# Optimization experiments

Measured on AMD Instinct MI355X. Metric: run time of the kernel, lower is better.

The kernel has to match this reference:

```python
import jax, jax.numpy as jnp
import numpy as np


def _lstm_layer(x, W_ih, W_hh, b_ih, b_hh, reverse=False):
    """Single LSTM layer. x: [T, B, D] -> outputs [T, B, H]. PyTorch gate order i,f,g,o."""
    H = W_hh.shape[-1]
    B = x.shape[1]
    # precompute input contribution for all steps
    xg = jnp.einsum('tbd,gd->tbg', x, W_ih) + b_ih + b_hh  # [T, B, 4H]

    def step(carry, xt):
        h, c = carry
        gates = xt + h @ W_hh.T
        i, f, g, o = jnp.split(gates, 4, axis=-1)
        c = jax.nn.sigmoid(f) * c + jax.nn.sigmoid(i) * jnp.tanh(g)
        h = jax.nn.sigmoid(o) * jnp.tanh(c)
        return (h, c), h

    init = (jnp.zeros((B, H), x.dtype), jnp.zeros((B, H), x.dtype))
    _, hs = jax.lax.scan(step, init, xg, reverse=reverse)
    return hs


def setup_inputs() -> dict:
    key = jax.random.key(0)
    ks = jax.random.split(key, 24)
    B, S, L = 64, 256, 16
    VOCAB, CVOCAB, NCLS = 50000, 128, 50
    E, CE, H = 100, 50, 300
    IN0 = E + CE          # 150, bilstm layer-0 input
    IN1 = 2 * H           # 600, bilstm layer-1 input

    def u(k, shape, fan):
        lim = 1.0 / np.sqrt(fan)
        return jax.random.uniform(k, shape, jnp.float32, -lim, lim)

    inp = {
        'word_ids': jax.random.randint(ks[0], (B, S), 0, VOCAB, jnp.int32),
        'char_ids': jax.random.randint(ks[1], (B, S, L), 0, CVOCAB, jnp.int32),
        'word_embed': jax.random.normal(ks[2], (VOCAB, E), jnp.float32) * 0.1,
        'char_embed': jax.random.normal(ks[3], (CVOCAB, CE), jnp.float32) * 0.1,
        # char LSTM: 2 layers, unidirectional, input==hidden==CE -> stack over layers
        'cWih': u(ks[4], (2, 4 * CE, CE), CE),
        'cWhh': u(ks[5], (2, 4 * CE, CE), CE),
        'cbih': u(ks[6], (2, 4 * CE), CE),
        'cbhh': u(ks[7], (2, 4 * CE), CE),
        # bilstm layer 0: stack over directions [2, ...]
        'b0_Wih': u(ks[8], (2, 4 * H, IN0), H),
        'b0_Whh': u(ks[9], (2, 4 * H, H), H),
        'b0_bih': u(ks[10], (2, 4 * H), H),
        'b0_bhh': u(ks[11], (2, 4 * H), H),
        # bilstm layer 1
        'b1_Wih': u(ks[12], (2, 4 * H, IN1), H),
        'b1_Whh': u(ks[13], (2, 4 * H, H), H),
        'b1_bih': u(ks[14], (2, 4 * H), H),
        'b1_bhh': u(ks[15], (2, 4 * H), H),
        'fcW': u(ks[16], (NCLS, 2 * H), 2 * H),
        'fcb': u(ks[17], (NCLS,), 2 * H),
    }
    return inp


def reference(word_ids, char_ids, word_embed, char_embed, cWih, cWhh, cbih, cbhh,
              b0_Wih, b0_Whh, b0_bih, b0_bhh, b1_Wih, b1_Whh, b1_bih, b1_bhh,
              fcW, fcb):
    B, S, L = char_ids.shape
    CE = char_embed.shape[1]

    # --- char-level path: batch all B*S words through the 2-layer char LSTM ---
    ch = char_embed[char_ids.reshape(B * S, L)]            # [BS, L, CE]
    x = jnp.transpose(ch, (1, 0, 2))                       # [L, BS, CE]
    x = _lstm_layer(x, cWih[0], cWhh[0], cbih[0], cbhh[0])
    x = _lstm_layer(x, cWih[1], cWhh[1], cbih[1], cbhh[1])
    char_feat = x[-1].reshape(B, S, CE)                    # last step of top layer

    # --- word path + concat ---
    emb = word_embed[word_ids]                             # [B, S, E]
    seq = jnp.transpose(jnp.concatenate([emb, char_feat], axis=-1), (1, 0, 2))  # [S, B, 150]

    # --- 2-layer bidirectional LSTM ---
    f0 = _lstm_layer(seq, b0_Wih[0], b0_Whh[0], b0_bih[0], b0_bhh[0])
    r0 = _lstm_layer(seq, b0_Wih[1], b0_Whh[1], b0_bih[1], b0_bhh[1], reverse=True)
    h0 = jnp.concatenate([f0, r0], axis=-1)                # [S, B, 600]
    f1 = _lstm_layer(h0, b1_Wih[0], b1_Whh[0], b1_bih[0], b1_bhh[0])
    r1 = _lstm_layer(h0, b1_Wih[1], b1_Whh[1], b1_bih[1], b1_bhh[1], reverse=True)
    h1 = jnp.concatenate([f1, r1], axis=-1)                # [S, B, 600]

    out = jnp.einsum('sbh,ch->bsc', h1, fcW) + fcb         # [B, S, NCLS]
    return jax.nn.log_softmax(out, axis=-1)
```

## Files before the change

### kernel.cpp

```cpp
#include <hip/hip_runtime.h>

typedef unsigned short u16;
typedef unsigned int   u32;
typedef unsigned long long u64;
typedef __attribute__((ext_vector_type(8))) short bf16x8;
typedef __attribute__((ext_vector_type(4))) float f32x4;

#define MFMA16(a,b,c) __builtin_amdgcn_mfma_f32_16x16x32_bf16((a),(b),(c),0,0,0)

#define NWG   19
#define HP    320
#define GP    304
#define XGB   4096
#define SLOTS 257
#define HSLOT 20480

static const size_t OFF_XG  = 0;
static const size_t SZ_XG   = (size_t)2*256*NWG*XGB*2;
static const size_t OFF_H0  = OFF_XG + SZ_XG;
static const size_t SZ_HB   = (size_t)2*SLOTS*HSLOT*2;
static const size_t OFF_H1  = OFF_H0 + SZ_HB;
static const size_t OFF_CF  = OFF_H1 + SZ_HB;
static const size_t SZ_CF   = (size_t)16384*64*2;
static const size_t OFF_W0  = OFF_CF + SZ_CF;
static const size_t SZ_W0   = (size_t)2432*160*2;
static const size_t OFF_W1  = OFF_W0 + SZ_W0;
static const size_t SZ_W1   = (size_t)2432*640*2;
static const size_t OFF_WFC = OFF_W1 + SZ_W1;
static const size_t SZ_WFC  = (size_t)64*640*2;
static const size_t OFF_B0  = OFF_WFC + SZ_WFC;
static const size_t OFF_B1  = OFF_B0 + 2432*4;
static const size_t OFF_BFC = OFF_B1 + 2432*4;
static const size_t OFF_DT  = OFF_BFC + 64*4;
static const size_t WS_NEED = OFF_DT + 4;

__device__ __forceinline__ float bf2f(u16 u){ union{u32 i; float f;} v; v.i=(u32)u<<16; return v.f; }
__device__ __forceinline__ u16 f2bf(float f){ union{float f; u32 u;} v; v.f=f; u32 r=v.u+0x7fffu+((v.u>>16)&1u); return (u16)(r>>16); }
__device__ __forceinline__ float sigf(float x){ return __builtin_amdgcn_rcpf(1.f+__builtin_amdgcn_exp2f(-1.4426950408889634f*x)); }
__device__ __forceinline__ float tanhf_(float x){ return 2.f*__builtin_amdgcn_rcpf(1.f+__builtin_amdgcn_exp2f(-2.8853900817779268f*x))-1.f; }
__device__ __forceinline__ float ldf(const void* p, size_t i, bool f32){
  return f32 ? ((const float*)p)[i] : bf2f(((const u16*)p)[i]);
}
__device__ __forceinline__ u16 ldh(const void* p, size_t i, bool f32){
  return f32 ? f2bf(((const float*)p)[i]) : ((const u16*)p)[i];
}

__global__ __launch_bounds__(256,1) void k_detect(const u16* __restrict__ probe, u32* __restrict__ cnt)
{
  int c = 0;
  for (int i = threadIdx.x; i < 65536; i += 256) {
    u16 v = probe[i];
    if (((v >> 7) & 0xFF) == 0xFF) ++c;
  }
  if (c) atomicAdd(cnt, (u32)c);
}

__global__ __launch_bounds__(256,4) void k_prep(
    const void* __restrict__ b0_Wih, const void* __restrict__ b0_bih, const void* __restrict__ b0_bhh,
    const void* __restrict__ b1_Wih, const void* __restrict__ b1_bih, const void* __restrict__ b1_bhh,
    const void* __restrict__ fcW,    const void* __restrict__ fcb,
    u16* __restrict__ W0p, u16* __restrict__ W1p, u16* __restrict__ Wfc,
    float* __restrict__ bias0, float* __restrict__ bias1, float* __restrict__ biasfc,
    const u32* __restrict__ dtf)
{
  const bool isf32 = (*dtf >= 8u);
  const int T0 = 2432*160, T1 = 2432*640, T2 = 64*640;
  const int total = T0 + T1 + T2 + 2432 + 2432 + 64;
  for (int i = blockIdx.x*256 + threadIdx.x; i < total; i += gridDim.x*256) {
    int x = i;
    if (x < T0) {
      int n = x/160, k = x%160;
      int dir = n/1216, cc = n%1216, g = cc/GP, uu = cc%GP;
      W0p[x] = (uu<300 && k<150) ? ldh(b0_Wih, ((size_t)dir*1200 + g*300 + uu)*150 + k, isf32) : (u16)0;
      continue;
    }
    x -= T0;
    if (x < T1) {
      int n = x/640, k = x%640;
      int dir = n/1216, cc = n%1216, g = cc/GP, uu = cc%GP;
      int part = (k>=320), ui = k - part*320;
      W1p[x] = (uu<300 && ui<300) ? ldh(b1_Wih, ((size_t)dir*1200 + g*300 + uu)*600 + part*300 + ui, isf32) : (u16)0;
      continue;
    }
    x -= T1;
    if (x < T2) {
      int n = x/640, k = x%640;
      int part = (k>=320), ui = k - part*320;
      Wfc[x] = (n<50 && ui<300) ? ldh(fcW, (size_t)n*600 + part*300 + ui, isf32) : (u16)0;
      continue;
    }
    x -= T2;
    if (x < 2432) {
      int dir = x/1216, cc = x%1216, g = cc/GP, uu = cc%GP;
      bias0[x] = (uu<300) ? ldf(b0_bih, dir*1200+g*300+uu, isf32) + ldf(b0_bhh, dir*1200+g*300+uu, isf32) : 0.f;
      continue;
    }
    x -= 2432;
    if (x < 2432) {
      int dir = x/1216, cc = x%1216, g = cc/GP, uu = cc%GP;
      bias1[x] = (uu<300) ? ldf(b1_bih, dir*1200+g*300+uu, isf32) + ldf(b1_bhh, dir*1200+g*300+uu, isf32) : 0.f;
      continue;
    }
    x -= 2432;
    biasfc[x] = (x<50) ? ldf(fcb, x, isf32) : 0.f;
  }
}

__global__ __launch_bounds__(256,1) void k_char(
    const int* __restrict__ char_ids, const void* __restrict__ cemb,
    const void* __restrict__ cWih, const void* __restrict__ cWhh,
    const void* __restrict__ cbih, const void* __restrict__ cbhh,
    u16* __restrict__ charfeat, const u32* __restrict__ dtf)
{
  __shared__ u16 emb[128][64];
  __shared__ int ids[16][64];
  __shared__ u16 h0s[64][72];
  __shared__ u16 h1s[64][72];
  const bool isf32 = (*dtf >= 8u);
  const int tid = threadIdx.x;
  const int g0  = blockIdx.x * 64;

  for (int e = tid; e < 128*64; e += 256) {
    int row = e>>6, col = e&63;
    (&emb[0][0])[e] = (col<50) ? ldh(cemb, row*50 + col, isf32) : (u16)0;
  }
  for (int e = tid; e < 1024; e += 256) ids[e&15][e>>4] = char_ids[(size_t)g0*16 + e];
  for (int e = tid; e < 4096; e += 256) { h0s[e>>6][e&63] = 0; h1s[e>>6][e&63] = 0; }
  __syncthreads();

  const int w = tid>>6, lane = tid&63, quad = lane>>4, lcol = lane&15;
  const int u = w*16 + lcol;

  bf16x8 Wf[2][4][4];
  #pragma unroll
  for (int l=0; l<2; ++l)
    #pragma unroll
    for (int g=0; g<4; ++g)
      #pragma unroll
      for (int kt=0; kt<4; ++kt) {
        union { bf16x8 v; u16 h[8]; } t8;
        #pragma unroll
        for (int q=0; q<8; ++q) {
          int k = kt*32 + quad*8 + q;
          u16 val = 0;
          if (u < 50) {
            if (k < 50)                  val = ldh(cWih, l*10000 + (g*50+u)*50 + k, isf32);
            else if (k >= 64 && k < 114) val = ldh(cWhh, l*10000 + (g*50+u)*50 + (k-64), isf32);
          }
          t8.h[q] = val;
        }
        Wf[l][g][kt] = t8.v;
      }
  float bs[2][4];
  #pragma unroll
  for (int l=0; l<2; ++l)
    #pragma unroll
    for (int g=0; g<4; ++g)
      bs[l][g] = (u<50) ? ldf(cbih, l*200+g*50+u, isf32) + ldf(cbhh, l*200+g*50+u, isf32) : 0.f;

  float c0[4][4] = {}; float c1[4][4] = {};
  float h0n[4][4], h1n[4][4];

  for (int t=0; t<16; ++t) {
    #pragma unroll
    for (int m=0; m<4; ++m) {
      f32x4 acc[4];
      #pragma unroll
      for (int g=0; g<4; ++g) acc[g] = (f32x4){bs[0][g], bs[0][g], bs[0][g], bs[0][g]};
      #pragma unroll
      for (int kt=0; kt<4; ++kt) {
        bf16x8 a;
        if (kt < 2) { int id = ids[t][m*16+lcol]; a = *(const bf16x8*)&emb[id][kt*32 + quad*8]; }
        else        { a = *(const bf16x8*)&h0s[m*16+lcol][(kt-2)*32 + quad*8]; }
        #pragma unroll
        for (int g=0; g<4; ++g) acc[g] = MFMA16(a, Wf[0][g][kt], acc[g]);
      }
      #pragma unroll
      for (int r=0; r<4; ++r) {
        float cn = sigf(acc[1][r])*c0[m][r] + sigf(acc[0][r])*tanhf_(acc[2][r]);
        c0[m][r] = cn;
        h0n[m][r] = sigf(acc[3][r]) * tanhf_(cn);
      }
    }
    __syncthreads();
    #pragma unroll
    for (int m=0; m<4; ++m)
      #pragma unroll
      for (int r=0; r<4; ++r) h0s[m*16 + quad*4 + r][u] = f2bf(h0n[m][r]);
    __syncthreads();
    #pragma unroll
    for (int m=0; m<4; ++m) {
      f32x4 acc[4];
      #pragma unroll
      for (int g=0; g<4; ++g) acc[g] = (f32x4){bs[1][g], bs[1][g], bs[1][g], bs[1][g]};
      #pragma unroll
      for (int kt=0; kt<4; ++kt) {
        bf16x8 a = (kt<2) ? *(const bf16x8*)&h0s[m*16+lcol][kt*32 + quad*8]
                          : *(const bf16x8*)&h1s[m*16+lcol][(kt-2)*32 + quad*8];
        #pragma unroll
        for (int g=0; g<4; ++g) acc[g] = MFMA16(a, Wf[1][g][kt], acc[g]);
      }
      #pragma unroll
      for (int r=0; r<4; ++r) {
        float cn = sigf(acc[1][r])*c1[m][r] + sigf(acc[0][r])*tanhf_(acc[2][r]);
        c1[m][r] = cn;
        h1n[m][r] = sigf(acc[3][r]) * tanhf_(cn);
      }
    }
    __syncthreads();
    #pragma unroll
    for (int m=0; m<4; ++m)
      #pragma unroll
      for (int r=0; r<4; ++r) h1s[m*16 + quad*4 + r][u] = f2bf(h1n[m][r]);
    __syncthreads();
  }
  for (int e = tid; e < 4096; e += 256)
    charfeat[(size_t)(g0 + (e>>6))*64 + (e&63)] = h1s[e>>6][e&63];
}

__device__ __forceinline__ size_t xg_addr(int n, int row){
  int dir = n/1216, cc = n%1216, g = cc/GP, cg = cc%GP, jj = cg>>4, uc = cg&15;
  int t = row>>6, b = row&63;
  size_t off = ((size_t)(g*4 + (b>>4))*64 + ((b>>2)&3)*16 + uc)*4 + (b&3);
  return (((size_t)dir*256 + t)*NWG + jj)*XGB + off;
}

__global__ __launch_bounds__(256,2) void k_proj0(
    const int* __restrict__ word_ids, const void* __restrict__ wemb,
    const u16* __restrict__ charfeat, const u16* __restrict__ W0p,
    const float* __restrict__ bias0, u16* __restrict__ xg, const u32* __restrict__ dtf)
{
  __shared__ u16 As[64][160];
  __shared__ u16 Bst[64][160];
  const bool isf32 = (*dtf >= 8u);
  const int tid = threadIdx.x;
  const int r0 = blockIdx.x*64, n0 = blockIdx.y*64;
  u32* Asu = (u32*)&As[0][0];
  u32* Bsu = (u32*)&Bst[0][0];
  for (int e = tid; e < 64*80; e += 256) {
    int rr = e/80, cu = e%80;
    int r = r0 + rr, t = r>>6, b = r&63;
    u32 v;
    if (cu < 50) {
      int wid = word_ids[b*256 + t];
      if (isf32) {
        const float* wf = (const float*)wemb;
        v = (u32)f2bf(wf[(size_t)wid*100 + cu*2]) | ((u32)f2bf(wf[(size_t)wid*100 + cu*2 + 1]) << 16);
      } else {
        v = ((const u32*)wemb)[(size_t)wid*50 + cu];
      }
    }
    else if (cu < 75) { v = ((const u32*)charfeat)[(size_t)r*32 + (cu-50)]; }
    else              v = 0;
    Asu[rr*80 + cu] = v;
  }
  for (int e = tid; e < 64*80; e += 256) {
    int n = e/80, cu = e%80;
    Bsu[n*80 + cu] = ((const u32*)W0p)[(size_t)(n0+n)*80 + cu];
  }
  __syncthreads();
  const int w = tid>>6, lane = tid&63, quad = lane>>4, lcol = lane&15;
  f32x4 acc[4] = {};
  #pragma unroll
  for (int kt=0; kt<5; ++kt) {
    bf16x8 a = *(const bf16x8*)&As[w*16+lcol][kt*32 + quad*8];
    #pragma unroll
    for (int nt=0; nt<4; ++nt) {
      bf16x8 bb = *(const bf16x8*)&Bst[nt*16+lcol][kt*32 + quad*8];
      acc[nt] = MFMA16(a, bb, acc[nt]);
    }
  }
  #pragma unroll
  for (int nt=0; nt<4; ++nt) {
    int n = n0 + nt*16 + lcol;
    float bia = bias0[n];
    #pragma unroll
    for (int r=0; r<4; ++r) {
      int row = r0 + w*16 + quad*4 + r;
      xg[xg_addr(n, row)] = f2bf(acc[nt][r] + bia);
    }
  }
}

__global__ __launch_bounds__(256,2) void k_proj1(
    const u16* __restrict__ Hbuf, const u16* __restrict__ W1p,
    const float* __restrict__ bias1, u16* __restrict__ xg)
{
  __shared__ u16 As[64][128];
  __shared__ u16 Bst[64][128];
  const int tid = threadIdx.x;
  const int r0 = blockIdx.x*64, n0 = blockIdx.y*64;
  const u32* Hu = (const u32*)Hbuf;
  const u32* Wu = (const u32*)W1p;
  u32* Asu = (u32*)&As[0][0];
  u32* Bsu = (u32*)&Bst[0][0];
  const int w = tid>>6, lane = tid&63, quad = lane>>4, lcol = lane&15;
  f32x4 acc[4] = {};
  for (int ch=0; ch<5; ++ch) {
    __syncthreads();
    for (int e = tid; e < 4096; e += 256) {
      int rr = e>>6, cu = e&63;
      int r = r0 + rr, t = r>>6, b = r&63;
      int kk = ch*128 + cu*2;
      int part = (kk>=320), uu = kk - part*320;
      u32 v = 0;
      if (uu < 304) {
        size_t slot = part ? (size_t)(256 - t) : (size_t)(t + 1);
        v = Hu[(size_t)part*SLOTS*10240 + slot*10240 + ((size_t)(uu>>5)*64 + b)*16 + ((uu&31)>>1)];
      }
      Asu[e] = v;
    }
    for (int e = tid; e < 4096; e += 256) {
      int n = e>>6, cu = e&63;
      Bsu[e] = Wu[(size_t)(n0+n)*320 + ch*64 + cu];
    }
    __syncthreads();
    #pragma unroll
    for (int kt=0; kt<4; ++kt) {
      bf16x8 a = *(const bf16x8*)&As[w*16+lcol][kt*32 + quad*8];
      #pragma unroll
      for (int nt=0; nt<4; ++nt) {
        bf16x8 bb = *(const bf16x8*)&Bst[nt*16+lcol][kt*32 + quad*8];
        acc[nt] = MFMA16(a, bb, acc[nt]);
      }
    }
  }
  #pragma unroll
  for (int nt=0; nt<4; ++nt) {
    int n = n0 + nt*16 + lcol;
    float bia = bias1[n];
    #pragma unroll
    for (int r=0; r<4; ++r) {
      int row = r0 + w*16 + quad*4 + r;
      xg[xg_addr(n, row)] = f2bf(acc[nt][r] + bia);
    }
  }
}

__global__ __launch_bounds__(256,1) void k_scan(
    const u16* __restrict__ xg, const void* __restrict__ Whh,
    u16* __restrict__ Hbuf, const u32* __restrict__ dtf)
{
  const bool isf32 = (*dtf >= 8u);
  const int bx = blockIdx.x;
  const int d = bx / NWG, j = bx % NWG;
  const int tid = threadIdx.x;
  const int w = tid>>6, lane = tid&63, quad = lane>>4, lcol = lane&15;
  const int u = j*16 + lcol;
  const int brow = w*16;
  const int ktj = j>>1, kub = (j&1)*16;

  bf16x8 Bf[4][10];
  #pragma unroll
  for (int g=0; g<4; ++g)
    #pragma unroll
    for (int kt=0; kt<10; ++kt) {
      union { bf16x8 v; u16 h[8]; } t8;
      #pragma unroll
      for (int q=0; q<8; ++q) {
        int k = kt*32 + quad*8 + q;
        t8.h[q] = (u < 300 && k < 300) ? ldh(Whh, ((size_t)d*1200 + g*300 + u)*300 + k, isf32) : (u16)0;
      }
      Bf[g][kt] = t8.v;
    }

  float c[4] = {0.f,0.f,0.f,0.f};
  const bool okq = (quad < 2);

  for (int t=0; t<256; ++t) {
    const int tt = d ? (255 - t) : t;
    const u64* xp = (const u64*)(xg + (((size_t)d*256 + tt)*NWG + j)*XGB);
    u64 xq[4];
    #pragma unroll
    for (int g=0; g<4; ++g) xq[g] = xp[(g*4 + w)*64 + lane];

    union HU { bf16x8 v; u64 q[2]; u32 w4[4]; };
    HU a[10];
    const u64* hp = (const u64*)Hbuf + (((size_t)d*SLOTS + t)*HSLOT >> 2);
    while (true) {
      #pragma unroll
      for (int kt=0; kt<9; ++kt) {
        size_t bi = (size_t)(kt*64 + brow + lcol)*8 + quad*2;
        a[kt].q[0] = __hip_atomic_load(hp + bi,     __ATOMIC_RELAXED, __HIP_MEMORY_SCOPE_AGENT);
        a[kt].q[1] = __hip_atomic_load(hp + bi + 1, __ATOMIC_RELAXED, __HIP_MEMORY_SCOPE_AGENT);
      }
      if (okq) {
        size_t bi = (size_t)(9*64 + brow + lcol)*8 + quad*2;
        a[9].q[0] = __hip_atomic_load(hp + bi,     __ATOMIC_RELAXED, __HIP_MEMORY_SCOPE_AGENT);
        a[9].q[1] = __hip_atomic_load(hp + bi + 1, __ATOMIC_RELAXED, __HIP_MEMORY_SCOPE_AGENT);
      } else { a[9].q[0] = 0; a[9].q[1] = 0; }
      u32 mx = 0u;
      #pragma unroll
      for (int kt=0; kt<10; ++kt)
        #pragma unroll
        for (int i=0; i<4; ++i) { u32 ww = a[kt].w4[i]; mx = (ww > mx) ? ww : mx; }
      if (__ballot(mx != 0xFFFFFFFFu) == ~0ull) break;
      __builtin_amdgcn_s_sleep(1);
    }

    f32x4 acc[4];
    #pragma unroll
    for (int g=0; g<4; ++g) {
      union { u64 q; u16 h[4]; } t4; t4.q = xq[g];
      #pragma unroll
      for (int r=0; r<4; ++r) acc[g][r] = bf2f(t4.h[r]);
    }
    #pragma unroll
    for (int kt=0; kt<10; ++kt) {
      #pragma unroll
      for (int g=0; g<4; ++g) acc[g] = MFMA16(a[kt].v, Bf[g][kt], acc[g]);
    }
    size_t sbase = ((size_t)d*SLOTS + (t+1))*HSLOT;
    #pragma unroll
    for (int r=0; r<4; ++r) {
      float cn = sigf(acc[1][r])*c[r] + sigf(acc[0][r])*tanhf_(acc[2][r]);
      c[r] = cn;
      float h = sigf(acc[3][r]) * tanhf_(cn);
      u32 mine = (u32)f2bf(h);
      u32 other = (u32)__shfl_xor((int)mine, 1, 64);
      if ((lcol & 1) == 0) {
        u32 word = mine | (other << 16);
        int b = brow + quad*4 + r;
        size_t e = sbase + (size_t)(ktj*64 + b)*32 + kub + lcol;
        __hip_atomic_store((u32*)(Hbuf + e), word, __ATOMIC_RELAXED, __HIP_MEMORY_SCOPE_AGENT);
      }
    }
  }
}

__global__ __launch_bounds__(256,2) void k_fc(
    const u16* __restrict__ Hbuf, const u16* __restrict__ Wfc,
    const float* __restrict__ biasfc, void* __restrict__ outv, const u32* __restrict__ dtf)
{
  __shared__ u16 As[64][128];
  __shared__ u16 Bst[64][128];
  const bool isf32 = (*dtf >= 8u);
  const int tid = threadIdx.x;
  const int r0 = blockIdx.x*64;
  const u32* Hu = (const u32*)Hbuf;
  const u32* Wu = (const u32*)Wfc;
  u32* Asu = (u32*)&As[0][0];
  u32* Bsu = (u32*)&Bst[0][0];
  const int w = tid>>6, lane = tid&63, quad = lane>>4, lcol = lane&15;
  f32x4 acc[4] = {};
  for (int ch=0; ch<5; ++ch) {
    __syncthreads();
    for (int e = tid; e < 4096; e += 256) {
      int rr = e>>6, cu = e&63;
      int r = r0 + rr, t = r>>6, b = r&63;
      int kk = ch*128 + cu*2;
      int part = (kk>=320), uu = kk - part*320;
      u32 v = 0;
      if (uu < 304) {
        size_t slot = part ? (size_t)(256 - t) : (size_t)(t + 1);
        v = Hu[(size_t)part*SLOTS*10240 + slot*10240 + ((size_t)(uu>>5)*64 + b)*16 + ((uu&31)>>1)];
      }
      Asu[e] = v;
    }
    for (int e = tid; e < 4096; e += 256) {
      int n = e>>6, cu = e&63;
      Bsu[e] = Wu[(size_t)n*320 + ch*64 + cu];
    }
    __syncthreads();
    #pragma unroll
    for (int kt=0; kt<4; ++kt) {
      bf16x8 a = *(const bf16x8*)&As[w*16+lcol][kt*32 + quad*8];
      #pragma unroll
      for (int nt=0; nt<4; ++nt) {
        bf16x8 bb = *(const bf16x8*)&Bst[nt*16+lcol][kt*32 + quad*8];
        acc[nt] = MFMA16(a, bb, acc[nt]);
      }
    }
  }
  float vals[4][4];
  #pragma unroll
  for (int nt=0; nt<4; ++nt) {
    int cc = nt*16 + lcol;
    float bia = biasfc[cc];
    #pragma unroll
    for (int r=0; r<4; ++r) vals[nt][r] = (cc < 50) ? (acc[nt][r] + bia) : -3.0e38f;
  }
  float lz[4];
  #pragma unroll
  for (int r=0; r<4; ++r) {
    float m = fmaxf(fmaxf(vals[0][r], vals[1][r]), fmaxf(vals[2][r], vals[3][r]));
    #pragma unroll
    for (int dd=1; dd<16; dd<<=1) m = fmaxf(m, __shfl_xor(m, dd, 64));
    float s = 0.f;
    #pragma unroll
    for (int nt=0; nt<4; ++nt) s += __builtin_amdgcn_exp2f((vals[nt][r]-m)*1.4426950408889634f);
    #pragma unroll
    for (int dd=1; dd<16; dd<<=1) s += __shfl_xor(s, dd, 64);
    lz[r] = m + __builtin_amdgcn_logf(s)*0.6931471805599453f;
  }
  #pragma unroll
  for (int nt=0; nt<4; ++nt) {
    int cc = nt*16 + lcol;
    if (cc < 50) {
      #pragma unroll
      for (int r=0; r<4; ++r) {
        int row = r0 + w*16 + quad*4 + r;
        int t = row>>6, b = row&63;
        size_t idx = ((size_t)b*256 + t)*50 + cc;
        float v = vals[nt][r] - lz[r];
        if (isf32) ((float*)outv)[idx] = v;
        else       ((u16*)outv)[idx] = f2bf(v);
      }
    }
  }
}

extern "C" void kernel_launch(void* const* d_in, const int* in_sizes, int n_in,
                              void* d_out, int out_size, void* d_ws, size_t ws_size,
                              hipStream_t stream) {
  (void)in_sizes; (void)n_in; (void)out_size;
  if (ws_size < WS_NEED) return;

  const int* word_ids = (const int*)d_in[0];
  const int* char_ids = (const int*)d_in[1];
  const void* wemb   = d_in[2];
  const void* cemb   = d_in[3];
  const void* cWih   = d_in[4];
  const void* cWhh   = d_in[5];
  const void* cbih   = d_in[6];
  const void* cbhh   = d_in[7];
  const void* b0_Wih = d_in[8];
  const void* b0_Whh = d_in[9];
  const void* b0_bih = d_in[10];
  const void* b0_bhh = d_in[11];
  const void* b1_Wih = d_in[12];
  const void* b1_Whh = d_in[13];
  const void* b1_bih = d_in[14];
  const void* b1_bhh = d_in[15];
  const void* fcW    = d_in[16];
  const void* fcb    = d_in[17];

  char* ws = (char*)d_ws;
  u16*   xg   = (u16*)(ws + OFF_XG);
  u16*   H0   = (u16*)(ws + OFF_H0);
  u16*   H1   = (u16*)(ws + OFF_H1);
  u16*   cf   = (u16*)(ws + OFF_CF);
  u16*   W0p  = (u16*)(ws + OFF_W0);
  u16*   W1p  = (u16*)(ws + OFF_W1);
  u16*   Wfc  = (u16*)(ws + OFF_WFC);
  float* bia0 = (float*)(ws + OFF_B0);
  float* bia1 = (float*)(ws + OFF_B1);
  float* biaf = (float*)(ws + OFF_BFC);
  u32*   dtf  = (u32*)(ws + OFF_DT);

  hipMemsetAsync(H0, 0xFF, SZ_HB, stream);
  hipMemsetAsync(H1, 0xFF, SZ_HB, stream);
  hipMemsetAsync(H0,                      0, (size_t)HSLOT*2, stream);
  hipMemsetAsync(H0 + (size_t)SLOTS*HSLOT, 0, (size_t)HSLOT*2, stream);
  hipMemsetAsync(H1,                      0, (size_t)HSLOT*2, stream);
  hipMemsetAsync(H1 + (size_t)SLOTS*HSLOT, 0, (size_t)HSLOT*2, stream);
  hipMemsetAsync(dtf, 0, 4, stream);

  k_detect<<<1, 256, 0, stream>>>((const u16*)wemb, dtf);
  k_prep<<<7780, 256, 0, stream>>>(b0_Wih, b0_bih, b0_bhh, b1_Wih, b1_bih, b1_bhh,
                                   fcW, fcb, W0p, W1p, Wfc, bia0, bia1, biaf, dtf);
  k_char<<<256, 256, 0, stream>>>(char_ids, cemb, cWih, cWhh, cbih, cbhh, cf, dtf);
  k_proj0<<<dim3(256,38), 256, 0, stream>>>(word_ids, wemb, cf, W0p, bia0, xg, dtf);
  k_scan<<<2*NWG, 256, 0, stream>>>(xg, b0_Whh, H0, dtf);
  k_proj1<<<dim3(256,38), 256, 0, stream>>>(H0, W1p, bia1, xg);
  k_scan<<<2*NWG, 256, 0, stream>>>(xg, b1_Whh, H1, dtf);
  k_fc<<<256, 256, 0, stream>>>(H1, Wfc, biaf, d_out, dtf);
}
```

Measured before the change: 2.612 ms.

## Halve scan workgroups per direction, each computing 32 hidden units per step

The recurrent scan kernel now uses 10 workgroups per direction instead of 19, and each one computes two 16-unit slices of the hidden state, with the xg layout widened to match. This cuts the number of workgroups that must poll and synchronise through global memory every timestep and reuses each loaded h fragment across twice as many MFMAs. In exchange each workgroup holds twice the recurrent weights in registers and does twice the per-step compute, which lengthens the serial critical path. The spin-loop sleep is also removed, and the final k-tile is now loaded in full rather than only for the lower quads.

```diff
diff --git a/kernel.cpp b/kernel.cpp
--- a/kernel.cpp
+++ b/kernel.cpp
@@ -8,10 +8,9 @@
 
 #define MFMA16(a,b,c) __builtin_amdgcn_mfma_f32_16x16x32_bf16((a),(b),(c),0,0,0)
 
-#define NWG   19
-#define HP    320
+#define NWG   10
 #define GP    304
-#define XGB   4096
+#define XGB   8192
 #define SLOTS 257
 #define HSLOT 20480
 
@@ -219,9 +218,10 @@
 }
 
 __device__ __forceinline__ size_t xg_addr(int n, int row){
-  int dir = n/1216, cc = n%1216, g = cc/GP, cg = cc%GP, jj = cg>>4, uc = cg&15;
+  int dir = n/1216, cc = n%1216, g = cc/GP, cg = cc%GP;
+  int jj = cg>>5, s = (cg>>4)&1, uc = cg&15;
   int t = row>>6, b = row&63;
-  size_t off = ((size_t)(g*4 + (b>>4))*64 + ((b>>2)&3)*16 + uc)*4 + (b&3);
+  size_t off = ((size_t)((g*2+s)*4 + (b>>4))*64 + ((b>>2)&3)*16 + uc)*4 + (b&3);
   return (((size_t)dir*256 + t)*NWG + jj)*XGB + off;
 }
 
@@ -346,83 +346,88 @@
   const int d = bx / NWG, j = bx % NWG;
   const int tid = threadIdx.x;
   const int w = tid>>6, lane = tid&63, quad = lane>>4, lcol = lane&15;
-  const int u = j*16 + lcol;
   const int brow = w*16;
-  const int ktj = j>>1, kub = (j&1)*16;
-
-  bf16x8 Bf[4][10];
+
+  bf16x8 Bf[4][2][10];
   #pragma unroll
   for (int g=0; g<4; ++g)
     #pragma unroll
-    for (int kt=0; kt<10; ++kt) {
-      union { bf16x8 v; u16 h[8]; } t8;
-      #pragma unroll
-      for (int q=0; q<8; ++q) {
-        int k = kt*32 + quad*8 + q;
-        t8.h[q] = (u < 300 && k < 300) ? ldh(Whh, ((size_t)d*1200 + g*300 + u)*300 + k, isf32) : (u16)0;
-      }
-      Bf[g][kt] = t8.v;
-    }
-
-  float c[4] = {0.f,0.f,0.f,0.f};
-  const bool okq = (quad < 2);
+    for (int s=0; s<2; ++s)
+      #pragma unroll
+      for (int kt=0; kt<10; ++kt) {
+        const int u = j*32 + s*16 + lcol;
+        union { bf16x8 v; u16 h[8]; } t8;
+        #pragma unroll
+        for (int q=0; q<8; ++q) {
+          int k = kt*32 + quad*8 + q;
+          t8.h[q] = (u < 300 && k < 300) ? ldh(Whh, ((size_t)d*1200 + g*300 + u)*300 + k, isf32) : (u16)0;
+        }
+        Bf[g][s][kt] = t8.v;
+      }
+
+  float c[2][4] = {};
 
   for (int t=0; t<256; ++t) {
     const int tt = d ? (255 - t) : t;
     const u64* xp = (const u64*)(xg + (((size_t)d*256 + tt)*NWG + j)*XGB);
-    u64 xq[4];
-    #pragma unroll
-    for (int g=0; g<4; ++g) xq[g] = xp[(g*4 + w)*64 + lane];
+    u64 xq[4][2];
+    #pragma unroll
+    for (int g=0; g<4; ++g)
+      #pragma unroll
+      for (int s=0; s<2; ++s)
+        xq[g][s] = xp[((g*2+s)*4 + w)*64 + lane];
 
     union HU { bf16x8 v; u64 q[2]; u32 w4[4]; };
     HU a[10];
     const u64* hp = (const u64*)Hbuf + (((size_t)d*SLOTS + t)*HSLOT >> 2);
     while (true) {
       #pragma unroll
-      for (int kt=0; kt<9; ++kt) {
+      for (int kt=0; kt<10; ++kt) {
         size_t bi = (size_t)(kt*64 + brow + lcol)*8 + quad*2;
         a[kt].q[0] = __hip_atomic_load(hp + bi,     __ATOMIC_RELAXED, __HIP_MEMORY_SCOPE_AGENT);
         a[kt].q[1] = __hip_atomic_load(hp + bi + 1, __ATOMIC_RELAXED, __HIP_MEMORY_SCOPE_AGENT);
       }
-      if (okq) {
-        size_t bi = (size_t)(9*64 + brow + lcol)*8 + quad*2;
-        a[9].q[0] = __hip_atomic_load(hp + bi,     __ATOMIC_RELAXED, __HIP_MEMORY_SCOPE_AGENT);
-        a[9].q[1] = __hip_atomic_load(hp + bi + 1, __ATOMIC_RELAXED, __HIP_MEMORY_SCOPE_AGENT);
-      } else { a[9].q[0] = 0; a[9].q[1] = 0; }
       u32 mx = 0u;
       #pragma unroll
       for (int kt=0; kt<10; ++kt)
         #pragma unroll
         for (int i=0; i<4; ++i) { u32 ww = a[kt].w4[i]; mx = (ww > mx) ? ww : mx; }
       if (__ballot(mx != 0xFFFFFFFFu) == ~0ull) break;
-      __builtin_amdgcn_s_sleep(1);
-    }
-
-    f32x4 acc[4];
-    #pragma unroll
-    for (int g=0; g<4; ++g) {
-      union { u64 q; u16 h[4]; } t4; t4.q = xq[g];
-      #pragma unroll
-      for (int r=0; r<4; ++r) acc[g][r] = bf2f(t4.h[r]);
-    }
+    }
+
+    f32x4 acc[4][2];
+    #pragma unroll
+    for (int g=0; g<4; ++g)
+      #pragma unroll
+      for (int s=0; s<2; ++s) {
+        union { u64 q; u16 h[4]; } t4; t4.q = xq[g][s];
+        #pragma unroll
+        for (int r=0; r<4; ++r) acc[g][s][r] = bf2f(t4.h[r]);
+      }
     #pragma unroll
     for (int kt=0; kt<10; ++kt) {
       #pragma unroll
-      for (int g=0; g<4; ++g) acc[g] = MFMA16(a[kt].v, Bf[g][kt], acc[g]);
+      for (int g=0; g<4; ++g) {
+        acc[g][0] = MFMA16(a[kt].v, Bf[g][0][kt], acc[g][0]);
+        acc[g][1] = MFMA16(a[kt].v, Bf[g][1][kt], acc[g][1]);
+      }
     }
     size_t sbase = ((size_t)d*SLOTS + (t+1))*HSLOT;
     #pragma unroll
-    for (int r=0; r<4; ++r) {
-      float cn = sigf(acc[1][r])*c[r] + sigf(acc[0][r])*tanhf_(acc[2][r]);
-      c[r] = cn;
-      float h = sigf(acc[3][r]) * tanhf_(cn);
-      u32 mine = (u32)f2bf(h);
-      u32 other = (u32)__shfl_xor((int)mine, 1, 64);
-      if ((lcol & 1) == 0) {
-        u32 word = mine | (other << 16);
-        int b = brow + quad*4 + r;
-        size_t e = sbase + (size_t)(ktj*64 + b)*32 + kub + lcol;
-        __hip_atomic_store((u32*)(Hbuf + e), word, __ATOMIC_RELAXED, __HIP_MEMORY_SCOPE_AGENT);
+    for (int s=0; s<2; ++s) {
+      #pragma unroll
+      for (int r=0; r<4; ++r) {
+        float cn = sigf(acc[1][s][r])*c[s][r] + sigf(acc[0][s][r])*tanhf_(acc[2][s][r]);
+        c[s][r] = cn;
+        float h = sigf(acc[3][s][r]) * tanhf_(cn);
+        u32 mine = (u32)f2bf(h);
+        u32 other = (u32)__shfl_xor((int)mine, 1, 64);
+        if ((lcol & 1) == 0) {
+          u32 word = mine | (other << 16);
+          int b = brow + quad*4 + r;
+          size_t e = sbase + (size_t)(j*64 + b)*32 + s*16 + lcol;
+          __hip_atomic_store((u32*)(Hbuf + e), word, __ATOMIC_RELAXED, __HIP_MEMORY_SCOPE_AGENT);
+        }
       }
     }
   }
```

Result: slower. 2.839 ms (+8.7%).
